# Optimization experiments

Measured on AMD Instinct MI355X. Metric: run time of the kernel, lower is better.

## Reference

```python
import jax, jax.numpy as jnp
import numpy as np

EMBED_DIM = 1024
NUM_HEADS = 16
HEAD_DIM = EMBED_DIM // NUM_HEADS


def setup_inputs() -> dict:
    key = jax.random.key(0)
    ks = jax.random.split(key, 9)
    B, L, D = 4, 2048, EMBED_DIM
    s = 1.0 / np.sqrt(D)
    return {
        "inputs": jax.random.normal(ks[0], (B, L, D), dtype=jnp.float32),
        "wq": jax.random.normal(ks[1], (D, D), dtype=jnp.float32) * s,
        "bq": jax.random.normal(ks[2], (D,), dtype=jnp.float32) * s,
        "wk": jax.random.normal(ks[3], (D, D), dtype=jnp.float32) * s,
        "bk": jax.random.normal(ks[4], (D,), dtype=jnp.float32) * s,
        "wv": jax.random.normal(ks[5], (D, D), dtype=jnp.float32) * s,
        "bv": jax.random.normal(ks[6], (D,), dtype=jnp.float32) * s,
        "wo": jax.random.normal(ks[7], (D, D), dtype=jnp.float32) * s,
        "bo": jax.random.normal(ks[8], (D,), dtype=jnp.float32) * s,
    }


def reference(inputs, wq, bq, wk, bk, wv, bv, wo, bo):
    B, L, D = inputs.shape
    H, Hd = NUM_HEADS, HEAD_DIM
    # Linear projections (torch Linear: x @ W^T + b)
    q = inputs @ wq.T + bq
    k = inputs @ wk.T + bk
    v = inputs @ wv.T + bv
    # (B, L, D) -> (B, H, L, Hd)
    q = q.reshape(B, L, H, Hd).transpose(0, 2, 1, 3)
    k = k.reshape(B, L, H, Hd).transpose(0, 2, 1, 3)
    v = v.reshape(B, L, H, Hd).transpose(0, 2, 1, 3)
    scale = 1.0 / np.sqrt(Hd).astype(np.float32)
    scores = jnp.einsum("bhqd,bhkd->bhqk", q, k) * scale  # (B,H,L,L)
    attn = jax.nn.softmax(scores, axis=-1)
    out = jnp.einsum("bhqk,bhkd->bhqd", attn, v)  # (B,H,L,Hd)
    out = out.transpose(0, 2, 1, 3).reshape(B, L, D)
    return out @ wo.T + bo
```

## Files before the change

### kernel.cpp

```cpp
#include <hip/hip_runtime.h>

typedef __attribute__((ext_vector_type(8))) short short8;
typedef __attribute__((ext_vector_type(8))) unsigned short ushort8;
typedef __attribute__((ext_vector_type(4))) unsigned short ushort4_t;
typedef __attribute__((ext_vector_type(4))) unsigned u32x4;
typedef __attribute__((ext_vector_type(4))) float f32x4;
typedef __attribute__((ext_vector_type(16))) float f32x16;

#define GLOAD_LDS(gp, lp) \
  __builtin_amdgcn_global_load_lds((const __attribute__((address_space(1))) void*)(gp), \
                                   (__attribute__((address_space(3))) void*)(lp), 16, 0, 0)

static __device__ __forceinline__ unsigned short f2bf(float f) {
  unsigned int u = __float_as_uint(f);
  u = u + 0x7fffu + ((u >> 16) & 1u);
  return (unsigned short)(u >> 16);
}

static __device__ __forceinline__ float exp2i(float x) {
  float r;
  asm("v_exp_f32 %0, %1" : "=v"(r) : "v"(x));
  return r;
}

static __device__ __forceinline__ unsigned cvtpk(float a, float b) {
  unsigned r;
  asm("v_cvt_pk_bf16_f32 %0, %1, %2" : "=v"(r) : "v"(a), "v"(b));
  return r;
}

static __device__ __forceinline__ void pl32swap(unsigned& a, unsigned& b) {
  asm("v_permlane32_swap_b32 %0, %1" : "+v"(a), "+v"(b));
}

__global__ __launch_bounds__(256) void cvt_all(const float* __restrict__ X,
                                               const float* __restrict__ w0, const float* __restrict__ w1,
                                               const float* __restrict__ w2, const float* __restrict__ w3,
                                               unsigned short* __restrict__ Xb,
                                               unsigned short* __restrict__ o0, unsigned short* __restrict__ o1,
                                               unsigned short* __restrict__ o2, unsigned short* __restrict__ o3) {
  int bid = blockIdx.x;
  const float* in;
  unsigned short* out;
  int i;
  if (bid < 4096) {
    in = X; out = Xb; i = bid * 2048 + threadIdx.x * 8;
  } else {
    int idx = bid - 4096;
    int w = idx >> 9;
    in = (w == 0) ? w0 : (w == 1) ? w1 : (w == 2) ? w2 : w3;
    out = (w == 0) ? o0 : (w == 1) ? o1 : (w == 2) ? o2 : o3;
    i = (idx & 511) * 2048 + threadIdx.x * 8;
  }
  const float4* p = reinterpret_cast<const float4*>(in + i);
  float4 a = p[0], b = p[1];
  ushort8 o;
  o[0] = f2bf(a.x); o[1] = f2bf(a.y); o[2] = f2bf(a.z); o[3] = f2bf(a.w);
  o[4] = f2bf(b.x); o[5] = f2bf(b.y); o[6] = f2bf(b.z); o[7] = f2bf(b.w);
  *reinterpret_cast<ushort8*>(out + i) = o;
}

template <int MODE>
__global__ __launch_bounds__(256) void gemm_bt(const unsigned short* __restrict__ A,
                                               const unsigned short* __restrict__ B,
                                               const float* __restrict__ bias,
                                               void* __restrict__ Cptr,
                                               int M, int N, int K, float scale) {
  __shared__ char As[2][16384];
  __shared__ char Bs[2][16384];
  const int t = threadIdx.x;
  const int lane = t & 63, wave = t >> 6;
  const int wm = wave >> 1, wn = wave & 1;
  const int m0 = blockIdx.y * 128, n0 = blockIdx.x * 128;

  const unsigned short* aS[4];
  const unsigned short* bS[4];
#pragma unroll
  for (int j = 0; j < 4; j++) {
    int i = wave * 256 + j * 64 + lane;
    int r = i >> 3, c = ((i & 7) ^ (r & 7)) << 3;
    aS[j] = A + (size_t)(m0 + r) * K + c;
    bS[j] = B + (size_t)(n0 + r) * K + c;
  }

  f32x4 acc[4][4] = {};
  const int NT = K >> 6;

#pragma unroll
  for (int j = 0; j < 4; j++) {
    GLOAD_LDS(aS[j], As[0] + wave * 4096 + j * 1024);
    GLOAD_LDS(bS[j], Bs[0] + wave * 4096 + j * 1024);
  }

  for (int kt = 0; kt < NT; kt++) {
    const int cur = kt & 1;
    __syncthreads();
    if (kt + 1 < NT) {
      int ko = (kt + 1) << 6;
#pragma unroll
      for (int j = 0; j < 4; j++) {
        GLOAD_LDS(aS[j] + ko, As[cur ^ 1] + wave * 4096 + j * 1024);
        GLOAD_LDS(bS[j] + ko, Bs[cur ^ 1] + wave * 4096 + j * 1024);
      }
    }
    const char* Ac = As[cur];
    const char* Bc = Bs[cur];
#pragma unroll
    for (int ks = 0; ks < 2; ks++) {
      short8 af[4], bfr[4];
#pragma unroll
      for (int x = 0; x < 4; x++) {
        int arow = wm * 64 + x * 16 + (lane & 15);
        int kk = ks * 32 + (lane >> 4) * 8;
        af[x] = *reinterpret_cast<const short8*>(Ac + (((arow * 64 + kk) * 2) ^ ((arow & 7) << 4)));
        int brow = wn * 64 + x * 16 + (lane & 15);
        bfr[x] = *reinterpret_cast<const short8*>(Bc + (((brow * 64 + kk) * 2) ^ ((brow & 7) << 4)));
      }
      __builtin_amdgcn_s_setprio(1);
#pragma unroll
      for (int mi = 0; mi < 4; mi++)
#pragma unroll
        for (int ni = 0; ni < 4; ni++)
          acc[mi][ni] = __builtin_amdgcn_mfma_f32_16x16x32_bf16(af[mi], bfr[ni], acc[mi][ni], 0, 0, 0);
      __builtin_amdgcn_s_setprio(0);
    }
  }

#pragma unroll
  for (int mi = 0; mi < 4; mi++) {
#pragma unroll
    for (int ni = 0; ni < 4; ni++) {
      int n = n0 + wn * 64 + ni * 16 + (lane & 15);
      float bs = bias[n];
      int mbase = m0 + wm * 64 + mi * 16 + ((lane >> 4) << 2);
      if (MODE == 2) {
        int b = mbase >> 11, l = mbase & 2047;
        ushort4_t o;
#pragma unroll
        for (int r = 0; r < 4; r++) o[r] = f2bf(acc[mi][ni][r] + bs);
        *reinterpret_cast<ushort4_t*>((unsigned short*)Cptr + (size_t)(b * N + n) * 2048 + l) = o;
      } else if (MODE == 0) {
#pragma unroll
        for (int r = 0; r < 4; r++)
          ((unsigned short*)Cptr)[(size_t)(mbase + r) * N + n] = f2bf((acc[mi][ni][r] + bs) * scale);
      } else {
#pragma unroll
        for (int r = 0; r < 4; r++)
          ((float*)Cptr)[(size_t)(mbase + r) * N + n] = acc[mi][ni][r] + bs;
      }
    }
  }
}

__global__ __launch_bounds__(256, 4) void attn_fwd(const unsigned short* __restrict__ Q,
                                                   const unsigned short* __restrict__ Kb,
                                                   const unsigned short* __restrict__ Vt,
                                                   unsigned short* __restrict__ O) {
  const int orig = blockIdx.x;
  const int wgid = (orig & 7) * 128 + (orig >> 3);
  const int qt = wgid & 15;
  const int h = (wgid >> 4) & 15;
  const int b = wgid >> 8;
  const int q0 = qt * 128;

  __shared__ char Ks[2][8192];
  __shared__ char Vs[2][8192];
  const int t = threadIdx.x, lane = t & 63, wave = t >> 6;
  const int ql = lane & 31;
  const int hi = lane >> 5;
  const int qrow = q0 + wave * 32 + ql;
  const int sw = (ql & 7) << 4;

  int lo_[4];
#pragma unroll
  for (int st = 0; st < 4; st++) lo_[st] = (ql * 128 + sw) ^ (st * 32 + hi * 16);

  const int ic0 = wave * 128 + lane, ic1 = ic0 + 64;
  const int r0 = ic0 >> 3, c0 = ((ic0 & 7) ^ (r0 & 7)) << 3;
  const int r1 = ic1 >> 3, c1 = ((ic1 & 7) ^ (r1 & 7)) << 3;
  const unsigned short* kS0 = Kb + (size_t)(b * 2048 + r0) * 1024 + h * 64 + c0;
  const unsigned short* kS1 = Kb + (size_t)(b * 2048 + r1) * 1024 + h * 64 + c1;
  const unsigned short* vS0 = Vt + ((size_t)(b * 16 + h) * 64 + r0) * 2048 + c0;
  const unsigned short* vS1 = Vt + ((size_t)(b * 16 + h) * 64 + r1) * 2048 + c1;

  short8 qf[4];
  {
    const unsigned short* qp = Q + (size_t)(b * 2048 + qrow) * 1024 + h * 64 + hi * 8;
#pragma unroll
    for (int st = 0; st < 4; st++) qf[st] = *reinterpret_cast<const short8*>(qp + st * 16);
  }

  float l_run = 0.f;
  f32x16 accd0 = {}, accd1 = {};

  GLOAD_LDS(kS0, Ks[0] + wave * 2048);
  GLOAD_LDS(kS1, Ks[0] + wave * 2048 + 1024);
  GLOAD_LDS(vS0, Vs[0] + wave * 2048);
  GLOAD_LDS(vS1, Vs[0] + wave * 2048 + 1024);

#pragma unroll 2
  for (int kt = 0; kt < 32; kt++) {
    const int cur = kt & 1;
    __syncthreads();
    if (kt + 1 < 32) {
      size_t ko = (size_t)(kt + 1) * 65536;
      int vo = (kt + 1) * 64;
      GLOAD_LDS(kS0 + ko, Ks[cur ^ 1] + wave * 2048);
      GLOAD_LDS(kS1 + ko, Ks[cur ^ 1] + wave * 2048 + 1024);
      GLOAD_LDS(vS0 + vo, Vs[cur ^ 1] + wave * 2048);
      GLOAD_LDS(vS1 + vo, Vs[cur ^ 1] + wave * 2048 + 1024);
    }
    const char* Kc = Ks[cur];
    const char* Vc = Vs[cur];

    f32x16 s0 = {}, s1 = {};
    __builtin_amdgcn_s_setprio(1);
#pragma unroll
    for (int st = 0; st < 4; st++) {
      short8 k0 = *reinterpret_cast<const short8*>(Kc + lo_[st]);
      short8 k1 = *reinterpret_cast<const short8*>(Kc + lo_[st] + 4096);
      s0 = __builtin_amdgcn_mfma_f32_32x32x16_bf16(k0, qf[st], s0, 0, 0, 0);
      s1 = __builtin_amdgcn_mfma_f32_32x32x16_bf16(k1, qf[st], s1, 0, 0, 0);
    }
    __builtin_amdgcn_s_setprio(0);

    short8 pf0, pf1, pf2, pf3;
    float rs;
    {
#pragma unroll
      for (int r = 0; r < 16; r++) s0[r] = exp2i(s0[r]);
      float a0 = (s0[0] + s0[1]) + (s0[2] + s0[3]);
      float a1 = (s0[4] + s0[5]) + (s0[6] + s0[7]);
      float a2 = (s0[8] + s0[9]) + (s0[10] + s0[11]);
      float a3 = (s0[12] + s0[13]) + (s0[14] + s0[15]);
      rs = (a0 + a1) + (a2 + a3);
      unsigned w0 = cvtpk(s0[0], s0[1]), w1 = cvtpk(s0[2], s0[3]);
      unsigned w2 = cvtpk(s0[4], s0[5]), w3 = cvtpk(s0[6], s0[7]);
      pl32swap(w0, w2); pl32swap(w1, w3);
      u32x4 p0 = {w0, w1, w2, w3};
      pf0 = __builtin_bit_cast(short8, p0);
      unsigned w4 = cvtpk(s0[8], s0[9]), w5 = cvtpk(s0[10], s0[11]);
      unsigned w6 = cvtpk(s0[12], s0[13]), w7 = cvtpk(s0[14], s0[15]);
      pl32swap(w4, w6); pl32swap(w5, w7);
      u32x4 p1 = {w4, w5, w6, w7};
      pf1 = __builtin_bit_cast(short8, p1);
    }
    {
#pragma unroll
      for (int r = 0; r < 16; r++) s1[r] = exp2i(s1[r]);
      float a0 = (s1[0] + s1[1]) + (s1[2] + s1[3]);
      float a1 = (s1[4] + s1[5]) + (s1[6] + s1[7]);
      float a2 = (s1[8] + s1[9]) + (s1[10] + s1[11]);
      float a3 = (s1[12] + s1[13]) + (s1[14] + s1[15]);
      rs += (a0 + a1) + (a2 + a3);
      unsigned x0 = cvtpk(s1[0], s1[1]), x1 = cvtpk(s1[2], s1[3]);
      unsigned x2 = cvtpk(s1[4], s1[5]), x3 = cvtpk(s1[6], s1[7]);
      pl32swap(x0, x2); pl32swap(x1, x3);
      u32x4 p2 = {x0, x1, x2, x3};
      pf2 = __builtin_bit_cast(short8, p2);
      unsigned x4 = cvtpk(s1[8], s1[9]), x5 = cvtpk(s1[10], s1[11]);
      unsigned x6 = cvtpk(s1[12], s1[13]), x7 = cvtpk(s1[14], s1[15]);
      pl32swap(x4, x6); pl32swap(x5, x7);
      u32x4 p3 = {x4, x5, x6, x7};
      pf3 = __builtin_bit_cast(short8, p3);
    }
    l_run += rs;

    __builtin_amdgcn_s_setprio(1);
#pragma unroll
    for (int st = 0; st < 4; st++) {
      short8 pb = (st == 0) ? pf0 : (st == 1) ? pf1 : (st == 2) ? pf2 : pf3;
      short8 v0 = *reinterpret_cast<const short8*>(Vc + lo_[st]);
      short8 v1 = *reinterpret_cast<const short8*>(Vc + lo_[st] + 4096);
      accd0 = __builtin_amdgcn_mfma_f32_32x32x16_bf16(v0, pb, accd0, 0, 0, 0);
      accd1 = __builtin_amdgcn_mfma_f32_32x32x16_bf16(v1, pb, accd1, 0, 0, 0);
    }
    __builtin_amdgcn_s_setprio(0);
  }

  float l_tot = l_run + __shfl_xor(l_run, 32);
  float inv = 1.0f / l_tot;
  unsigned short* op = O + (size_t)(b * 2048 + qrow) * 1024 + h * 64;
#pragma unroll
  for (int g = 0; g < 4; g++) {
    ushort4_t o0, o1;
#pragma unroll
    for (int j = 0; j < 4; j++) {
      o0[j] = f2bf(accd0[4 * g + j] * inv);
      o1[j] = f2bf(accd1[4 * g + j] * inv);
    }
    *reinterpret_cast<ushort4_t*>(op + 8 * g + 4 * hi) = o0;
    *reinterpret_cast<ushort4_t*>(op + 32 + 8 * g + 4 * hi) = o1;
  }
}

extern "C" void kernel_launch(void* const* d_in, const int* in_sizes, int n_in,
                              void* d_out, int out_size, void* d_ws, size_t ws_size,
                              hipStream_t stream) {
  const float* X = (const float*)d_in[0];
  const float* wq = (const float*)d_in[1];
  const float* bq = (const float*)d_in[2];
  const float* wk = (const float*)d_in[3];
  const float* bk = (const float*)d_in[4];
  const float* wv = (const float*)d_in[5];
  const float* bv = (const float*)d_in[6];
  const float* wo = (const float*)d_in[7];
  const float* bo = (const float*)d_in[8];

  char* ws = (char*)d_ws;
  const size_t MB = 1024 * 1024;
  unsigned short* Xb  = (unsigned short*)(ws + 0);
  unsigned short* Wqb = (unsigned short*)(ws + 16 * MB);
  unsigned short* Wkb = (unsigned short*)(ws + 18 * MB);
  unsigned short* Wvb = (unsigned short*)(ws + 20 * MB);
  unsigned short* Wob = (unsigned short*)(ws + 22 * MB);
  unsigned short* Qb  = (unsigned short*)(ws + 24 * MB);
  unsigned short* Kb  = (unsigned short*)(ws + 40 * MB);
  unsigned short* Vtb = (unsigned short*)(ws + 56 * MB);
  unsigned short* Ob  = (unsigned short*)(ws + 72 * MB);

  cvt_all<<<4096 + 4 * 512, 256, 0, stream>>>(X, wq, wk, wv, wo, Xb, Wqb, Wkb, Wvb, Wob);

  const float QSCALE = 0.125f * 1.4426950408889634f;
  dim3 gg(8, 64);
  gemm_bt<0><<<gg, 256, 0, stream>>>(Xb, Wqb, bq, Qb, 8192, 1024, 1024, QSCALE);
  gemm_bt<0><<<gg, 256, 0, stream>>>(Xb, Wkb, bk, Kb, 8192, 1024, 1024, 1.0f);
  gemm_bt<2><<<gg, 256, 0, stream>>>(Xb, Wvb, bv, Vtb, 8192, 1024, 1024, 1.0f);

  attn_fwd<<<1024, 256, 0, stream>>>(Qb, Kb, Vtb, Ob);

  gemm_bt<1><<<gg, 256, 0, stream>>>(Ob, Wob, bo, (float*)d_out, 8192, 1024, 1024, 1.0f);
}
```

Measured before the change: 194.1 us.

## Software-pipeline PV MFMA one tile behind QK with triple-buffered V

Restructures the attention loop so the P·V matrix multiply for the previous key tile is issued right after the current tile's Q·K MFMAs, before the softmax exponentials. This lets the exp/convert work overlap with tensor-core work. V gets a third LDS buffer because it must stay resident one iteration longer, and an epilogue handles the final tile. The cost is extra LDS use (which may reduce occupancy under launch_bounds(256,4)), more live registers for the carried P fragments, and the loss of the unroll-2 pragma.

```diff
diff --git a/kernel.cpp b/kernel.cpp
--- a/kernel.cpp
+++ b/kernel.cpp
@@ -164,7 +164,7 @@
   const int q0 = qt * 128;
 
   __shared__ char Ks[2][8192];
-  __shared__ char Vs[2][8192];
+  __shared__ char Vs[3][8192];
   const int t = threadIdx.x, lane = t & 63, wave = t >> 6;
   const int ql = lane & 31;
   const int hi = lane >> 5;
@@ -192,26 +192,29 @@
 
   float l_run = 0.f;
   f32x16 accd0 = {}, accd1 = {};
+  short8 pf0, pf1, pf2, pf3;
 
   GLOAD_LDS(kS0, Ks[0] + wave * 2048);
   GLOAD_LDS(kS1, Ks[0] + wave * 2048 + 1024);
   GLOAD_LDS(vS0, Vs[0] + wave * 2048);
   GLOAD_LDS(vS1, Vs[0] + wave * 2048 + 1024);
 
-#pragma unroll 2
+  int vpv = 0;
+  int vst = 8192;
+
   for (int kt = 0; kt < 32; kt++) {
-    const int cur = kt & 1;
     __syncthreads();
     if (kt + 1 < 32) {
       size_t ko = (size_t)(kt + 1) * 65536;
       int vo = (kt + 1) * 64;
-      GLOAD_LDS(kS0 + ko, Ks[cur ^ 1] + wave * 2048);
-      GLOAD_LDS(kS1 + ko, Ks[cur ^ 1] + wave * 2048 + 1024);
-      GLOAD_LDS(vS0 + vo, Vs[cur ^ 1] + wave * 2048);
-      GLOAD_LDS(vS1 + vo, Vs[cur ^ 1] + wave * 2048 + 1024);
-    }
-    const char* Kc = Ks[cur];
-    const char* Vc = Vs[cur];
+      char* kd = Ks[(kt + 1) & 1] + wave * 2048;
+      GLOAD_LDS(kS0 + ko, kd);
+      GLOAD_LDS(kS1 + ko, kd + 1024);
+      char* vd = Vs[0] + vst + wave * 2048;
+      GLOAD_LDS(vS0 + vo, vd);
+      GLOAD_LDS(vS1 + vo, vd + 1024);
+    }
+    const char* Kc = Ks[kt & 1];
 
     f32x16 s0 = {}, s1 = {};
     __builtin_amdgcn_s_setprio(1);
@@ -222,9 +225,20 @@
       s0 = __builtin_amdgcn_mfma_f32_32x32x16_bf16(k0, qf[st], s0, 0, 0, 0);
       s1 = __builtin_amdgcn_mfma_f32_32x32x16_bf16(k1, qf[st], s1, 0, 0, 0);
     }
+    if (kt > 0) {
+      const char* Vp = Vs[0] + vpv;
+#pragma unroll
+      for (int st = 0; st < 4; st++) {
+        short8 pb = (st == 0) ? pf0 : (st == 1) ? pf1 : (st == 2) ? pf2 : pf3;
+        short8 v0 = *reinterpret_cast<const short8*>(Vp + lo_[st]);
+        short8 v1 = *reinterpret_cast<const short8*>(Vp + lo_[st] + 4096);
+        accd0 = __builtin_amdgcn_mfma_f32_32x32x16_bf16(v0, pb, accd0, 0, 0, 0);
+        accd1 = __builtin_amdgcn_mfma_f32_32x32x16_bf16(v1, pb, accd1, 0, 0, 0);
+      }
+      vpv += 8192; if (vpv == 24576) vpv = 0;
+    }
     __builtin_amdgcn_s_setprio(0);
 
-    short8 pf0, pf1, pf2, pf3;
     float rs;
     {
 #pragma unroll
@@ -266,12 +280,17 @@
     }
     l_run += rs;
 
+    vst += 8192; if (vst == 24576) vst = 0;
+  }
+
+  {
+    const char* Vp = Vs[0] + vpv;
     __builtin_amdgcn_s_setprio(1);
 #pragma unroll
     for (int st = 0; st < 4; st++) {
       short8 pb = (st == 0) ? pf0 : (st == 1) ? pf1 : (st == 2) ? pf2 : pf3;
-      short8 v0 = *reinterpret_cast<const short8*>(Vc + lo_[st]);
-      short8 v1 = *reinterpret_cast<const short8*>(Vc + lo_[st] + 4096);
+      short8 v0 = *reinterpret_cast<const short8*>(Vp + lo_[st]);
+      short8 v1 = *reinterpret_cast<const short8*>(Vp + lo_[st] + 4096);
       accd0 = __builtin_amdgcn_mfma_f32_32x32x16_bf16(v0, pb, accd0, 0, 0, 0);
       accd1 = __builtin_amdgcn_mfma_f32_32x32x16_bf16(v1, pb, accd1, 0, 0, 0);
     }
```

Measured after the change: 193.5 us. No clear change (-0.3%).

## Use 256x128 tiles, 8 waves and triple-buffered LDS in projection GEMMs

Applied to the files above, without the earlier changes.

Replaces the 128x128 four-wave GEMM with a 256x128 tile run by 512 threads. It uses a three-stage LDS ring with explicit vmcnt waits and raw barriers, so two k-tiles are in flight while one is being computed. It also remaps block IDs so that consecutive blocks share A rows, and hardcodes K=N=1024. In exchange it uses 144KB of LDS per block, which allows only one block per CU, and it launches 256 blocks, which may underfill 256 CUs with no tail slack.

```diff
diff --git a/kernel.cpp b/kernel.cpp
--- a/kernel.cpp
+++ b/kernel.cpp
@@ -61,57 +61,70 @@
 }
 
 template <int MODE>
-__global__ __launch_bounds__(256) void gemm_bt(const unsigned short* __restrict__ A,
-                                               const unsigned short* __restrict__ B,
-                                               const float* __restrict__ bias,
-                                               void* __restrict__ Cptr,
-                                               int M, int N, int K, float scale) {
-  __shared__ char As[2][16384];
-  __shared__ char Bs[2][16384];
+__global__ __launch_bounds__(512) void gemm_bt8(const unsigned short* __restrict__ A,
+                                                const unsigned short* __restrict__ B,
+                                                const float* __restrict__ bias,
+                                                void* __restrict__ Cptr, float scale) {
+  const int K = 1024, N = 1024;
+  __shared__ char As[3][32768];
+  __shared__ char Bs[3][16384];
   const int t = threadIdx.x;
   const int lane = t & 63, wave = t >> 6;
   const int wm = wave >> 1, wn = wave & 1;
-  const int m0 = blockIdx.y * 128, n0 = blockIdx.x * 128;
+  const int orig = blockIdx.x;
+  const int wgid = (orig & 7) * 32 + (orig >> 3);
+  const int my = wgid >> 3, nx = wgid & 7;
+  const int m0 = my * 256, n0 = nx * 128;
 
   const unsigned short* aS[4];
-  const unsigned short* bS[4];
+  const unsigned short* bS[2];
 #pragma unroll
   for (int j = 0; j < 4; j++) {
-    int i = wave * 256 + j * 64 + lane;
+    int i = j * 512 + t;
     int r = i >> 3, c = ((i & 7) ^ (r & 7)) << 3;
     aS[j] = A + (size_t)(m0 + r) * K + c;
+  }
+#pragma unroll
+  for (int j = 0; j < 2; j++) {
+    int i = j * 512 + t;
+    int r = i >> 3, c = ((i & 7) ^ (r & 7)) << 3;
     bS[j] = B + (size_t)(n0 + r) * K + c;
   }
+  const int toff = t * 16;
 
   f32x4 acc[4][4] = {};
-  const int NT = K >> 6;
-
-#pragma unroll
-  for (int j = 0; j < 4; j++) {
-    GLOAD_LDS(aS[j], As[0] + wave * 4096 + j * 1024);
-    GLOAD_LDS(bS[j], Bs[0] + wave * 4096 + j * 1024);
-  }
-
-  for (int kt = 0; kt < NT; kt++) {
-    const int cur = kt & 1;
-    __syncthreads();
-    if (kt + 1 < NT) {
-      int ko = (kt + 1) << 6;
-#pragma unroll
-      for (int j = 0; j < 4; j++) {
-        GLOAD_LDS(aS[j] + ko, As[cur ^ 1] + wave * 4096 + j * 1024);
-        GLOAD_LDS(bS[j] + ko, Bs[cur ^ 1] + wave * 4096 + j * 1024);
-      }
+
+#pragma unroll
+  for (int j = 0; j < 4; j++) GLOAD_LDS(aS[j], As[0] + toff + j * 8192);
+#pragma unroll
+  for (int j = 0; j < 2; j++) GLOAD_LDS(bS[j], Bs[0] + toff + j * 8192);
+#pragma unroll
+  for (int j = 0; j < 4; j++) GLOAD_LDS(aS[j] + 64, As[1] + toff + j * 8192);
+#pragma unroll
+  for (int j = 0; j < 2; j++) GLOAD_LDS(bS[j] + 64, Bs[1] + toff + j * 8192);
+
+  int cur = 0, stg = 2;
+  for (int kt = 0; kt < 16; kt++) {
+    if (kt < 15) asm volatile("s_waitcnt vmcnt(6)" ::: "memory");
+    else         asm volatile("s_waitcnt vmcnt(0)" ::: "memory");
+    __builtin_amdgcn_s_barrier();
+    __builtin_amdgcn_sched_barrier(0);
+    if (kt + 2 < 16) {
+      int ko = (kt + 2) << 6;
+#pragma unroll
+      for (int j = 0; j < 4; j++) GLOAD_LDS(aS[j] + ko, As[stg] + toff + j * 8192);
+#pragma unroll
+      for (int j = 0; j < 2; j++) GLOAD_LDS(bS[j] + ko, Bs[stg] + toff + j * 8192);
     }
     const char* Ac = As[cur];
     const char* Bc = Bs[cur];
 #pragma unroll
     for (int ks = 0; ks < 2; ks++) {
       short8 af[4], bfr[4];
+      int kk = ks * 32 + (lane >> 4) * 8;
 #pragma unroll
       for (int x = 0; x < 4; x++) {
         int arow = wm * 64 + x * 16 + (lane & 15);
-        int kk = ks * 32 + (lane >> 4) * 8;
         af[x] = *reinterpret_cast<const short8*>(Ac + (((arow * 64 + kk) * 2) ^ ((arow & 7) << 4)));
         int brow = wn * 64 + x * 16 + (lane & 15);
         bfr[x] = *reinterpret_cast<const short8*>(Bc + (((brow * 64 + kk) * 2) ^ ((brow & 7) << 4)));
@@ -124,6 +137,8 @@
           acc[mi][ni] = __builtin_amdgcn_mfma_f32_16x16x32_bf16(af[mi], bfr[ni], acc[mi][ni], 0, 0, 0);
       __builtin_amdgcn_s_setprio(0);
     }
+    cur = (cur == 2) ? 0 : cur + 1;
+    stg = (stg == 2) ? 0 : stg + 1;
   }
 
 #pragma unroll
@@ -322,12 +337,11 @@
   cvt_all<<<4096 + 4 * 512, 256, 0, stream>>>(X, wq, wk, wv, wo, Xb, Wqb, Wkb, Wvb, Wob);
 
   const float QSCALE = 0.125f * 1.4426950408889634f;
-  dim3 gg(8, 64);
-  gemm_bt<0><<<gg, 256, 0, stream>>>(Xb, Wqb, bq, Qb, 8192, 1024, 1024, QSCALE);
-  gemm_bt<0><<<gg, 256, 0, stream>>>(Xb, Wkb, bk, Kb, 8192, 1024, 1024, 1.0f);
-  gemm_bt<2><<<gg, 256, 0, stream>>>(Xb, Wvb, bv, Vtb, 8192, 1024, 1024, 1.0f);
+  gemm_bt8<0><<<256, 512, 0, stream>>>(Xb, Wqb, bq, Qb, QSCALE);
+  gemm_bt8<0><<<256, 512, 0, stream>>>(Xb, Wkb, bk, Kb, 1.0f);
+  gemm_bt8<2><<<256, 512, 0, stream>>>(Xb, Wvb, bv, Vtb, 1.0f);
 
   attn_fwd<<<1024, 256, 0, stream>>>(Qb, Kb, Vtb, Ob);
 
-  gemm_bt<1><<<gg, 256, 0, stream>>>(Ob, Wob, bo, (float*)d_out, 8192, 1024, 1024, 1.0f);
-}
+  gemm_bt8<1><<<256, 512, 0, stream>>>(Ob, Wob, bo, (float*)d_out, 1.0f);
+}
```

After: 198.8 us. 1.02x slower.
